# Kernel tuning notes

Hardware: AMD Instinct MI355X
Metric: run time of the kernel (lower is better)

## Reference

```python
import jax, jax.numpy as jnp
import numpy as np

B, C, Q, E = 32, 1024, 128, 512

def setup_inputs() -> dict:
    key = jax.random.key(0)
    k1, k2, k3 = jax.random.split(key, 3)
    context = jax.random.normal(k1, (B, C, E), dtype=jnp.float32)
    question = jax.random.normal(k2, (B, Q, E), dtype=jnp.float32)
    # ws = [ws_q | ws_c | ws_m], matching cat([q, ctx, q*ctx]) order
    ws = jax.random.normal(k3, (3 * E,), dtype=jnp.float32) * (1.0 / np.sqrt(E))
    return {"context": context, "question": question, "ws": ws}

def reference(context, question, ws):
    ws_q, ws_c, ws_m = ws[:E], ws[E:2 * E], ws[2 * E:]
    # similarity[b,c,q] = ws_q.q[b,q] + ws_c.c[b,c] + ws_m.(q[b,q]*c[b,c])
    sim = (jnp.einsum('bqe,e->bq', question, ws_q)[:, None, :]
           + jnp.einsum('bce,e->bc', context, ws_c)[:, :, None]
           + jnp.einsum('bce,bqe,e->bcq', context, question, ws_m))  # (B,C,Q)
    c2q = jnp.einsum('bcq,bqe->bce', jax.nn.softmax(sim, axis=2), question)  # (B,C,E)
    q2c_w = jax.nn.softmax(jnp.max(sim, axis=2), axis=1)  # (B,C)
    q2c = jnp.einsum('bc,bce->be', q2c_w, context)[:, None, :]  # (B,1,E)
    return (c2q, q2c)
```

## Files before the change

### kernel.cpp

```cpp
#include <hip/hip_runtime.h>

#define BB 32
#define CC 1024
#define QQ 128
#define EE 512

typedef unsigned int uint32;
typedef unsigned short u16;
typedef __bf16 bf16x8 __attribute__((ext_vector_type(8)));
typedef float f32x4 __attribute__((ext_vector_type(4)));

#define QMF_OFF  (0u)
#define QTF_OFF  (4u<<20)
#define QDP_OFF  (8u<<20)
#define MB_OFF   ((8u<<20)+(192u<<10))
#define SB_OFF   ((8u<<20)+(200u<<10))
#define PVB_OFF  ((8u<<20)+(256u<<10))
#define P_OFF    (13u<<20)

__device__ __forceinline__ u16 bfc(float f){
  __bf16 h = (__bf16)f;
  return __builtin_bit_cast(u16, h);
}
__device__ __forceinline__ float bf2f(uint32 lo16){
  return __builtin_bit_cast(float, lo16 << 16);
}

__global__ __launch_bounds__(256) void k_prep(const float* __restrict__ q,
                                              const float* __restrict__ ws,
                                              unsigned char* __restrict__ wsp){
  const int b = blockIdx.x >> 2, et = blockIdx.x & 3, e0 = et*128;
  __shared__ u16 tm[128*136];
  __shared__ u16 tt[128*136];
  const int tid = threadIdx.x;
  float* qdp = (float*)(wsp + QDP_OFF) + (size_t)(b*4 + et)*128;
  #pragma unroll
  for (int i=0;i<16;i++){
    int id = tid + i*256;
    int qi = id >> 5;
    int el = (id & 31) << 2;
    float4 v = *(const float4*)(q + (size_t)(b*QQ+qi)*EE + e0 + el);
    float4 a = *(const float4*)(ws +          e0 + el);
    float4 c = *(const float4*)(ws +   EE +   e0 + el);
    float4 m = *(const float4*)(ws + 2*EE +   e0 + el);
    ushort4 um; um.x = bfc(v.x*m.x + c.x); um.y = bfc(v.y*m.y + c.y);
                um.z = bfc(v.z*m.z + c.z); um.w = bfc(v.w*m.w + c.w);
    *(ushort4*)&tm[qi*136 + el] = um;
    ushort4 ut; ut.x = bfc(v.x); ut.y = bfc(v.y); ut.z = bfc(v.z); ut.w = bfc(v.w);
    *(ushort4*)&tt[qi*136 + el] = ut;
    float d = v.x*a.x + v.y*a.y + v.z*a.z + v.w*a.w;
    d += __shfl_xor(d,1); d += __shfl_xor(d,2); d += __shfl_xor(d,4);
    d += __shfl_xor(d,8); d += __shfl_xor(d,16);
    if ((tid & 31) == 0) qdp[qi] = d;
  }
  __syncthreads();
  const int lane = tid & 63, wv = tid >> 6, l15 = lane & 15, l4 = lane >> 4;
  uint4* qmf = (uint4*)(wsp + QMF_OFF);
  uint4* qtf = (uint4*)(wsp + QTF_OFF);
  #pragma unroll
  for (int i=0;i<8;i++){
    int f = wv*8 + i;
    int kl = f >> 3, nf = f & 7;
    uint4 u = *(const uint4*)&tm[(nf*16 + l15)*136 + kl*32 + l4*8];
    qmf[(size_t)((b*16 + et*4 + kl)*8 + nf)*64 + lane] = u;
  }
  #pragma unroll
  for (int i=0;i<8;i++){
    int f = wv*8 + i;
    int ks2 = f >> 3, nl = f & 7, ne = et*8 + nl;
    uint32 x[4];
    #pragma unroll
    for (int p=0;p<4;p++){
      u16 t0 = tt[(ks2*32 + l4*8 + 2*p    )*136 + nl*16 + l15];
      u16 t1 = tt[(ks2*32 + l4*8 + 2*p + 1)*136 + nl*16 + l15];
      x[p] = (uint32)t0 | ((uint32)t1 << 16);
    }
    uint4 u; u.x = x[0]; u.y = x[1]; u.z = x[2]; u.w = x[3];
    qtf[(size_t)((b*4 + ks2)*32 + ne)*64 + lane] = u;
  }
}

__global__ __launch_bounds__(512, 4) void k_sim(const float* __restrict__ ctx,
                                                unsigned char* __restrict__ wsp){
  __shared__ __align__(16) unsigned char buf[32768];
  __shared__ float mx_s[16*8];
  __shared__ float sm_s[16*8];
  __shared__ float wrow_s[16];

  const int bid = blockIdx.x;
  const int sw  = (bid & 7)*256 + (bid >> 3);
  const int b   = sw >> 6;
  const int t   = sw & 63;
  const int tid = threadIdx.x;
  const int lane = tid & 63;
  const int w    = tid >> 6;
  const int l15  = lane & 15;
  const int l4   = lane >> 4;

  {
    const unsigned char* cb = (const unsigned char*)(ctx + (size_t)(b*CC + t*16)*EE);
    #pragma unroll
    for (int j=0;j<4;j++){
      const int chunk = w*4 + j;
      const int row   = chunk >> 1;
      const int gs    = ((chunk & 1)*64 + lane) ^ (row & 7);
      __builtin_amdgcn_global_load_lds(
        (const __attribute__((address_space(1))) uint32*)(cb + row*2048 + gs*16),
        (__attribute__((address_space(3))) uint32*)(buf + chunk*1024 + lane*16),
        16, 0, 0);
    }
  }

  float qdv[4];
  {
    const float* qdp = (const float*)(wsp + QDP_OFF) + (size_t)b*512;
    #pragma unroll
    for (int r=0;r<4;r++){
      const int qi = w*16 + l4*4 + r;
      qdv[r] = qdp[qi] + qdp[128+qi] + qdp[256+qi] + qdp[384+qi];
    }
  }
  __syncthreads();

  const uint4* qmf4 = (const uint4*)(wsp + QMF_OFF);
  f32x4 acc = (f32x4){0.f,0.f,0.f,0.f};
  {
    const int swz = l15 & 7;
    const unsigned char* rowb = buf + l15*2048;
    #pragma unroll
    for (int ks=0; ks<16; ks++){
      bf16x8 a = __builtin_bit_cast(bf16x8, qmf4[(size_t)((b*16 + ks)*8 + w)*64 + lane]);
      const int gs0 = ks*8 + l4*2;
      float4 x = *(const float4*)(rowb + ((gs0    ) ^ swz)*16);
      float4 y = *(const float4*)(rowb + ((gs0 + 1) ^ swz)*16);
      bf16x8 bf;
      bf[0]=(__bf16)x.x; bf[1]=(__bf16)x.y; bf[2]=(__bf16)x.z; bf[3]=(__bf16)x.w;
      bf[4]=(__bf16)y.x; bf[5]=(__bf16)y.y; bf[6]=(__bf16)y.z; bf[7]=(__bf16)y.w;
      acc = __builtin_amdgcn_mfma_f32_16x16x32_bf16(a, bf, acc, 0, 0, 0);
    }
  }

  float p[4];
  {
    float m = -3.0e38f, s = 0.f;
    #pragma unroll
    for (int r=0;r<4;r++){
      float vv = fminf(acc[r] + qdv[r], 80.f);
      m = fmaxf(m, vv);
      p[r] = __expf(vv);
      s += p[r];
    }
    m = fmaxf(m, __shfl_xor(m, 16)); m = fmaxf(m, __shfl_xor(m, 32));
    s += __shfl_xor(s, 16);          s += __shfl_xor(s, 32);
    if (l4 == 0){ mx_s[l15*8 + w] = m; sm_s[l15*8 + w] = s; }
  }
  __syncthreads();

  {
    const float* sp = &sm_s[l15*8];
    const float rden = 1.f/(sp[0]+sp[1]+sp[2]+sp[3]+sp[4]+sp[5]+sp[6]+sp[7]);
    u16 hb[4];
    #pragma unroll
    for (int r=0;r<4;r++) hb[r] = bfc(p[r]*rden);
    uint2 u; u.x = (uint32)hb[0] | ((uint32)hb[1]<<16);
             u.y = (uint32)hb[2] | ((uint32)hb[3]<<16);
    *(uint2*)(wsp + P_OFF
      + ((size_t)(b*64 + t)*4 + (w>>1))*1024
      + (((2*w + (l4>>1)) & 3)*16 + l15)*16 + (l4&1)*8) = u;
  }

  if (tid < 16){
    const float* mp = &mx_s[tid*8];
    float mf = fmaxf(fmaxf(fmaxf(mp[0],mp[1]),fmaxf(mp[2],mp[3])),
                     fmaxf(fmaxf(mp[4],mp[5]),fmaxf(mp[6],mp[7])));
    float M = mf;
    M = fmaxf(M, __shfl_xor(M,1)); M = fmaxf(M, __shfl_xor(M,2));
    M = fmaxf(M, __shfl_xor(M,4)); M = fmaxf(M, __shfl_xor(M,8));
    float wr = __expf(mf - M);
    wrow_s[tid] = wr;
    float S = wr;
    S += __shfl_xor(S,1); S += __shfl_xor(S,2);
    S += __shfl_xor(S,4); S += __shfl_xor(S,8);
    if (tid == 0){
      ((float*)(wsp + MB_OFF))[b*64 + t] = M;
      ((float*)(wsp + SB_OFF))[b*64 + t] = S;
    }
  }
  __syncthreads();

  {
    const int sl = tid >> 2, in = (tid & 3)*4;
    float pv = 0.f;
    #pragma unroll
    for (int rr=0; rr<16; rr++){
      float x = *(const float*)(buf + rr*2048 + ((sl ^ (rr & 7))*16) + in);
      pv = fmaf(wrow_s[rr], x, pv);
    }
    ((float*)(wsp + PVB_OFF))[(size_t)(b*64 + t)*512 + tid] = pv;
  }
}

__global__ __launch_bounds__(256, 4) void k_out(unsigned char* __restrict__ wsp,
                                                float* __restrict__ out){
  __shared__ __align__(16) unsigned char qts[32768];
  __shared__ float sc_s[64];
  __shared__ float dinv_s;

  const int bid = blockIdx.x;
  const int tid = threadIdx.x;

  if (bid >= 2048){
    const int b = bid - 2048;
    if (tid < 64){
      float Mk = ((const float*)(wsp + MB_OFF))[b*64 + tid];
      float Sk = ((const float*)(wsp + SB_OFF))[b*64 + tid];
      float M = Mk;
      M = fmaxf(M, __shfl_xor(M,1));  M = fmaxf(M, __shfl_xor(M,2));
      M = fmaxf(M, __shfl_xor(M,4));  M = fmaxf(M, __shfl_xor(M,8));
      M = fmaxf(M, __shfl_xor(M,16)); M = fmaxf(M, __shfl_xor(M,32));
      float ev = __expf(Mk - M);
      float d = ev*Sk;
      d += __shfl_xor(d,1);  d += __shfl_xor(d,2);  d += __shfl_xor(d,4);
      d += __shfl_xor(d,8);  d += __shfl_xor(d,16); d += __shfl_xor(d,32);
      sc_s[tid] = ev;
      if (tid == 0) dinv_s = 1.f/d;
    }
    __syncthreads();
    const float* pvb = (const float*)(wsp + PVB_OFF) + (size_t)b*64*512;
    float a0 = 0.f, a1 = 0.f;
    #pragma unroll 8
    for (int k=0;k<64;k++){
      float s = sc_s[k];
      a0 = fmaf(s, pvb[(size_t)k*512 + tid],       a0);
      a1 = fmaf(s, pvb[(size_t)k*512 + tid + 256], a1);
    }
    size_t base = (size_t)BB*CC*EE + (size_t)b*EE;
    float di = dinv_s;
    out[base + tid]       = a0*di;
    out[base + tid + 256] = a1*di;
    return;
  }

  const int sw  = (bid & 7)*256 + (bid >> 3);
  const int b   = sw >> 6;
  const int rr  = sw & 63;
  const int ct  = rr >> 2;
  const int et  = rr & 3;
  const int lane = tid & 63;
  const int w    = tid >> 6;
  const int l15  = lane & 15;
  const int l4   = lane >> 4;

  const unsigned char* qtfb = wsp + QTF_OFF + (size_t)b*131072;
  #pragma unroll
  for (int j=0;j<8;j++){
    __builtin_amdgcn_global_load_lds(
      (const __attribute__((address_space(1))) uint32*)
        (qtfb + (size_t)(w*32 + et*8 + j)*1024 + lane*16),
      (__attribute__((address_space(3))) uint32*)(qts + (w*8 + j)*1024), 16, 0, 0);
  }

  bf16x8 pa[4];
  #pragma unroll
  for (int k2=0;k2<4;k2++)
    pa[k2] = __builtin_bit_cast(bf16x8,
      *(const uint4*)(wsp + P_OFF + ((size_t)(b*64 + ct*4 + w)*4 + k2)*1024 + lane*16));
  __syncthreads();

  f32x4 acc2[8];
  #pragma unroll
  for (int n=0;n<8;n++) acc2[n] = (f32x4){0.f,0.f,0.f,0.f};
  #pragma unroll
  for (int k2=0;k2<4;k2++){
    #pragma unroll
    for (int n=0;n<8;n++){
      bf16x8 bq = __builtin_bit_cast(bf16x8,
        *(const uint4*)(qts + (k2*8 + n)*1024 + lane*16));
      acc2[n] = __builtin_amdgcn_mfma_f32_16x16x32_bf16(pa[k2], bq, acc2[n], 0, 0, 0);
    }
  }

  float* ob = out + (size_t)(b*CC + ct*64 + w*16)*EE + et*128;
  #pragma unroll
  for (int n=0;n<8;n++){
    #pragma unroll
    for (int r=0;r<4;r++)
      ob[(size_t)(l4*4 + r)*EE + n*16 + l15] = acc2[n][r];
  }
}

extern "C" void kernel_launch(void* const* d_in, const int* in_sizes, int n_in,
                              void* d_out, int out_size, void* d_ws, size_t ws_size,
                              hipStream_t stream){
  const float* ctx = (const float*)d_in[0];
  const float* q   = (const float*)d_in[1];
  const float* ws  = (const float*)d_in[2];
  float* out = (float*)d_out;
  unsigned char* wsp = (unsigned char*)d_ws;

  k_prep<<<dim3(BB*4),    dim3(256), 0, stream>>>(q, ws, wsp);
  k_sim <<<dim3(2048),    dim3(512), 0, stream>>>(ctx, wsp);
  k_out <<<dim3(2048+32), dim3(256), 0, stream>>>(wsp, out);
}
```

Baseline: 53.09 us.

## Fuse similarity and output kernels into a flag-synchronized persistent megakernel

Replaces the separate similarity and output kernels with one persistent kernel of 256 blocks. 128 producer blocks loop over 16 context tiles each, double-buffering context loads into LDS, and publish a flag for every 4 tiles. 128 consumer blocks spin on those flags and compute c2q tiles plus the q2c reduction as soon as their rows are ready. The goal is to overlap the two phases and remove a launch boundary. The cost is far fewer in-flight blocks, serialized per-block work, spin-wait overhead, and reliance on producers and consumers being co-resident; a new zeroing kernel resets the flags.

New measurement: 121.0 us. +127.9%, slower.

```diff
diff --git a/kernel.cpp b/kernel.cpp
--- a/kernel.cpp
+++ b/kernel.cpp
@@ -15,6 +15,7 @@
 #define QDP_OFF  (8u<<20)
 #define MB_OFF   ((8u<<20)+(192u<<10))
 #define SB_OFF   ((8u<<20)+(200u<<10))
+#define FLG_OFF  ((8u<<20)+(208u<<10))
 #define PVB_OFF  ((8u<<20)+(256u<<10))
 #define P_OFF    (13u<<20)
 
@@ -24,6 +25,13 @@
 }
 __device__ __forceinline__ float bf2f(uint32 lo16){
   return __builtin_bit_cast(float, lo16 << 16);
+}
+__device__ __forceinline__ void flag_set(uint32* f){
+  __hip_atomic_store(f, 1u, __ATOMIC_RELEASE, __HIP_MEMORY_SCOPE_AGENT);
+}
+__device__ __forceinline__ void flag_wait(uint32* f){
+  while (__hip_atomic_load(f, __ATOMIC_ACQUIRE, __HIP_MEMORY_SCOPE_AGENT) == 0u)
+    __builtin_amdgcn_s_sleep(8);
 }
 
 __global__ __launch_bounds__(256) void k_prep(const float* __restrict__ q,
@@ -80,212 +88,230 @@
   }
 }
 
-__global__ __launch_bounds__(512, 4) void k_sim(const float* __restrict__ ctx,
-                                                unsigned char* __restrict__ wsp){
-  __shared__ __align__(16) unsigned char buf[32768];
+__global__ __launch_bounds__(512) void k_zero(unsigned char* __restrict__ wsp){
+  flag_set((uint32*)(wsp + FLG_OFF) + threadIdx.x),
+  __hip_atomic_store((uint32*)(wsp + FLG_OFF) + threadIdx.x, 0u,
+                     __ATOMIC_RELEASE, __HIP_MEMORY_SCOPE_AGENT);
+}
+
+__global__ __launch_bounds__(512) void k_mega(const float* __restrict__ ctx,
+                                              unsigned char* __restrict__ wsp,
+                                              float* __restrict__ out){
+  __shared__ __align__(16) unsigned char mega[65536];
   __shared__ float mx_s[16*8];
   __shared__ float sm_s[16*8];
   __shared__ float wrow_s[16];
+  __shared__ float sc_s[64];
+  __shared__ float dinv_s;
 
   const int bid = blockIdx.x;
-  const int sw  = (bid & 7)*256 + (bid >> 3);
-  const int b   = sw >> 6;
-  const int t   = sw & 63;
   const int tid = threadIdx.x;
   const int lane = tid & 63;
   const int w    = tid >> 6;
   const int l15  = lane & 15;
   const int l4   = lane >> 4;
-
-  {
-    const unsigned char* cb = (const unsigned char*)(ctx + (size_t)(b*CC + t*16)*EE);
+  uint32* flags = (uint32*)(wsp + FLG_OFF);
+
+  if (bid < 128){
+    const int b   = bid >> 2;
+    const int q16 = (bid & 3) * 16;
+
+    const uint4* qmf4 = (const uint4*)(wsp + QMF_OFF);
+    bf16x8 a[16];
     #pragma unroll
-    for (int j=0;j<4;j++){
-      const int chunk = w*4 + j;
-      const int row   = chunk >> 1;
-      const int gs    = ((chunk & 1)*64 + lane) ^ (row & 7);
+    for (int ks=0;ks<16;ks++)
+      a[ks] = __builtin_bit_cast(bf16x8, qmf4[(size_t)((b*16 + ks)*8 + w)*64 + lane]);
+    float qdv[4];
+    {
+      const float* qdp = (const float*)(wsp + QDP_OFF) + (size_t)b*512;
+      #pragma unroll
+      for (int r=0;r<4;r++){
+        const int qi = w*16 + l4*4 + r;
+        qdv[r] = qdp[qi] + qdp[128+qi] + qdp[256+qi] + qdp[384+qi];
+      }
+    }
+
+    auto stage = [&](int t, unsigned char* dst){
+      const unsigned char* cb = (const unsigned char*)(ctx + (size_t)(b*CC + t*16)*EE);
+      #pragma unroll
+      for (int j=0;j<4;j++){
+        const int chunk = w*4 + j;
+        const int row   = chunk >> 1;
+        const int gs    = ((chunk & 1)*64 + lane) ^ (row & 7);
+        __builtin_amdgcn_global_load_lds(
+          (const __attribute__((address_space(1))) uint32*)(cb + row*2048 + gs*16),
+          (__attribute__((address_space(3))) uint32*)(dst + chunk*1024 + lane*16),
+          16, 0, 0);
+      }
+    };
+
+    stage(q16, mega);
+    __syncthreads();
+
+    for (int it=0; it<16; ++it){
+      const int t = q16 + it;
+      unsigned char* bufc = mega + (it & 1)*32768;
+      if (it < 15) stage(t+1, mega + ((it & 1)^1)*32768);
+
+      f32x4 acc = (f32x4){0.f,0.f,0.f,0.f};
+      {
+        const int swz = l15 & 7;
+        const unsigned char* rowb = bufc + l15*2048;
+        #pragma unroll
+        for (int ks=0; ks<16; ks++){
+          const int gs0 = ks*8 + l4*2;
+          float4 x = *(const float4*)(rowb + ((gs0    ) ^ swz)*16);
+          float4 y = *(const float4*)(rowb + ((gs0 + 1) ^ swz)*16);
+          bf16x8 bf;
+          bf[0]=(__bf16)x.x; bf[1]=(__bf16)x.y; bf[2]=(__bf16)x.z; bf[3]=(__bf16)x.w;
+          bf[4]=(__bf16)y.x; bf[5]=(__bf16)y.y; bf[6]=(__bf16)y.z; bf[7]=(__bf16)y.w;
+          acc = __builtin_amdgcn_mfma_f32_16x16x32_bf16(a[ks], bf, acc, 0, 0, 0);
+        }
+      }
+
+      float p[4];
+      {
+        float m = -3.0e38f, s = 0.f;
+        #pragma unroll
+        for (int r=0;r<4;r++){
+          float vv = fminf(acc[r] + qdv[r], 80.f);
+          m = fmaxf(m, vv);
+          p[r] = __expf(vv);
+          s += p[r];
+        }
+        m = fmaxf(m, __shfl_xor(m, 16)); m = fmaxf(m, __shfl_xor(m, 32));
+        s += __shfl_xor(s, 16);          s += __shfl_xor(s, 32);
+        if (l4 == 0){ mx_s[l15*8 + w] = m; sm_s[l15*8 + w] = s; }
+      }
+      __syncthreads();
+
+      {
+        const float* sp = &sm_s[l15*8];
+        const float rden = 1.f/(sp[0]+sp[1]+sp[2]+sp[3]+sp[4]+sp[5]+sp[6]+sp[7]);
+        u16 hb[4];
+        #pragma unroll
+        for (int r=0;r<4;r++) hb[r] = bfc(p[r]*rden);
+        uint2 u; u.x = (uint32)hb[0] | ((uint32)hb[1]<<16);
+                 u.y = (uint32)hb[2] | ((uint32)hb[3]<<16);
+        *(uint2*)(wsp + P_OFF
+          + ((size_t)(b*64 + t)*4 + (w>>1))*1024
+          + (((2*w + (l4>>1)) & 3)*16 + l15)*16 + (l4&1)*8) = u;
+      }
+
+      if (tid < 16){
+        const float* mp = &mx_s[tid*8];
+        float mf = fmaxf(fmaxf(fmaxf(mp[0],mp[1]),fmaxf(mp[2],mp[3])),
+                         fmaxf(fmaxf(mp[4],mp[5]),fmaxf(mp[6],mp[7])));
+        float M = mf;
+        M = fmaxf(M, __shfl_xor(M,1)); M = fmaxf(M, __shfl_xor(M,2));
+        M = fmaxf(M, __shfl_xor(M,4)); M = fmaxf(M, __shfl_xor(M,8));
+        float wr = __expf(mf - M);
+        wrow_s[tid] = wr;
+        float S = wr;
+        S += __shfl_xor(S,1); S += __shfl_xor(S,2);
+        S += __shfl_xor(S,4); S += __shfl_xor(S,8);
+        if (tid == 0){
+          ((float*)(wsp + MB_OFF))[b*64 + t] = M;
+          ((float*)(wsp + SB_OFF))[b*64 + t] = S;
+        }
+      }
+      __syncthreads();
+
+      {
+        const int sl = tid >> 2, in = (tid & 3)*4;
+        float pv = 0.f;
+        #pragma unroll
+        for (int rr=0; rr<16; rr++){
+          float x = *(const float*)(bufc + rr*2048 + ((sl ^ (rr & 7))*16) + in);
+          pv = fmaf(wrow_s[rr], x, pv);
+        }
+        ((float*)(wsp + PVB_OFF))[(size_t)(b*64 + t)*512 + tid] = pv;
+      }
+      __syncthreads();
+
+      if ((it & 3) == 3 && tid == 0)
+        flag_set(flags + b*16 + (t >> 2));
+    }
+  } else {
+    const int c    = bid - 128;
+    const int b    = c >> 2;
+    const int half = c & 1;
+    const int ep   = (c >> 1) & 1;
+    const int g    = w >> 2;
+    const int wv4  = w & 3;
+    const int et   = ep*2 + g;
+
+    const unsigned char* qtfb = wsp + QTF_OFF + (size_t)b*131072;
+    #pragma unroll
+    for (int j=0;j<8;j++){
       __builtin_amdgcn_global_load_lds(
-        (const __attribute__((address_space(1))) uint32*)(cb + row*2048 + gs*16),
-        (__attribute__((address_space(3))) uint32*)(buf + chunk*1024 + lane*16),
+        (const __attribute__((address_space(1))) uint32*)
+          (qtfb + (size_t)(wv4*32 + et*8 + j)*1024 + lane*16),
+        (__attribute__((address_space(3))) uint32*)(mega + g*32768 + (wv4*8 + j)*1024 + lane*16),
         16, 0, 0);
     }
-  }
-
-  float qdv[4];
-  {
-    const float* qdp = (const float*)(wsp + QDP_OFF) + (size_t)b*512;
-    #pragma unroll
-    for (int r=0;r<4;r++){
-      const int qi = w*16 + l4*4 + r;
-      qdv[r] = qdp[qi] + qdp[128+qi] + qdp[256+qi] + qdp[384+qi];
-    }
-  }
-  __syncthreads();
-
-  const uint4* qmf4 = (const uint4*)(wsp + QMF_OFF);
-  f32x4 acc = (f32x4){0.f,0.f,0.f,0.f};
-  {
-    const int swz = l15 & 7;
-    const unsigned char* rowb = buf + l15*2048;
-    #pragma unroll
-    for (int ks=0; ks<16; ks++){
-      bf16x8 a = __builtin_bit_cast(bf16x8, qmf4[(size_t)((b*16 + ks)*8 + w)*64 + lane]);
-      const int gs0 = ks*8 + l4*2;
-      float4 x = *(const float4*)(rowb + ((gs0    ) ^ swz)*16);
-      float4 y = *(const float4*)(rowb + ((gs0 + 1) ^ swz)*16);
-      bf16x8 bf;
-      bf[0]=(__bf16)x.x; bf[1]=(__bf16)x.y; bf[2]=(__bf16)x.z; bf[3]=(__bf16)x.w;
-      bf[4]=(__bf16)y.x; bf[5]=(__bf16)y.y; bf[6]=(__bf16)y.z; bf[7]=(__bf16)y.w;
-      acc = __builtin_amdgcn_mfma_f32_16x16x32_bf16(a, bf, acc, 0, 0, 0);
-    }
-  }
-
-  float p[4];
-  {
-    float m = -3.0e38f, s = 0.f;
-    #pragma unroll
-    for (int r=0;r<4;r++){
-      float vv = fminf(acc[r] + qdv[r], 80.f);
-      m = fmaxf(m, vv);
-      p[r] = __expf(vv);
-      s += p[r];
-    }
-    m = fmaxf(m, __shfl_xor(m, 16)); m = fmaxf(m, __shfl_xor(m, 32));
-    s += __shfl_xor(s, 16);          s += __shfl_xor(s, 32);
-    if (l4 == 0){ mx_s[l15*8 + w] = m; sm_s[l15*8 + w] = s; }
-  }
-  __syncthreads();
-
-  {
-    const float* sp = &sm_s[l15*8];
-    const float rden = 1.f/(sp[0]+sp[1]+sp[2]+sp[3]+sp[4]+sp[5]+sp[6]+sp[7]);
-    u16 hb[4];
-    #pragma unroll
-    for (int r=0;r<4;r++) hb[r] = bfc(p[r]*rden);
-    uint2 u; u.x = (uint32)hb[0] | ((uint32)hb[1]<<16);
-             u.y = (uint32)hb[2] | ((uint32)hb[3]<<16);
-    *(uint2*)(wsp + P_OFF
-      + ((size_t)(b*64 + t)*4 + (w>>1))*1024
-      + (((2*w + (l4>>1)) & 3)*16 + l15)*16 + (l4&1)*8) = u;
-  }
-
-  if (tid < 16){
-    const float* mp = &mx_s[tid*8];
-    float mf = fmaxf(fmaxf(fmaxf(mp[0],mp[1]),fmaxf(mp[2],mp[3])),
-                     fmaxf(fmaxf(mp[4],mp[5]),fmaxf(mp[6],mp[7])));
-    float M = mf;
-    M = fmaxf(M, __shfl_xor(M,1)); M = fmaxf(M, __shfl_xor(M,2));
-    M = fmaxf(M, __shfl_xor(M,4)); M = fmaxf(M, __shfl_xor(M,8));
-    float wr = __expf(mf - M);
-    wrow_s[tid] = wr;
-    float S = wr;
-    S += __shfl_xor(S,1); S += __shfl_xor(S,2);
-    S += __shfl_xor(S,4); S += __shfl_xor(S,8);
-    if (tid == 0){
-      ((float*)(wsp + MB_OFF))[b*64 + t] = M;
-      ((float*)(wsp + SB_OFF))[b*64 + t] = S;
-    }
-  }
-  __syncthreads();
-
-  {
-    const int sl = tid >> 2, in = (tid & 3)*4;
-    float pv = 0.f;
-    #pragma unroll
-    for (int rr=0; rr<16; rr++){
-      float x = *(const float*)(buf + rr*2048 + ((sl ^ (rr & 7))*16) + in);
-      pv = fmaf(wrow_s[rr], x, pv);
-    }
-    ((float*)(wsp + PVB_OFF))[(size_t)(b*64 + t)*512 + tid] = pv;
-  }
-}
-
-__global__ __launch_bounds__(256, 4) void k_out(unsigned char* __restrict__ wsp,
-                                                float* __restrict__ out){
-  __shared__ __align__(16) unsigned char qts[32768];
-  __shared__ float sc_s[64];
-  __shared__ float dinv_s;
-
-  const int bid = blockIdx.x;
-  const int tid = threadIdx.x;
-
-  if (bid >= 2048){
-    const int b = bid - 2048;
-    if (tid < 64){
-      float Mk = ((const float*)(wsp + MB_OFF))[b*64 + tid];
-      float Sk = ((const float*)(wsp + SB_OFF))[b*64 + tid];
-      float M = Mk;
-      M = fmaxf(M, __shfl_xor(M,1));  M = fmaxf(M, __shfl_xor(M,2));
-      M = fmaxf(M, __shfl_xor(M,4));  M = fmaxf(M, __shfl_xor(M,8));
-      M = fmaxf(M, __shfl_xor(M,16)); M = fmaxf(M, __shfl_xor(M,32));
-      float ev = __expf(Mk - M);
-      float d = ev*Sk;
-      d += __shfl_xor(d,1);  d += __shfl_xor(d,2);  d += __shfl_xor(d,4);
-      d += __shfl_xor(d,8);  d += __shfl_xor(d,16); d += __shfl_xor(d,32);
-      sc_s[tid] = ev;
-      if (tid == 0) dinv_s = 1.f/d;
-    }
     __syncthreads();
-    const float* pvb = (const float*)(wsp + PVB_OFF) + (size_t)b*64*512;
-    float a0 = 0.f, a1 = 0.f;
-    #pragma unroll 8
-    for (int k=0;k<64;k++){
-      float s = sc_s[k];
-      a0 = fmaf(s, pvb[(size_t)k*512 + tid],       a0);
-      a1 = fmaf(s, pvb[(size_t)k*512 + tid + 256], a1);
-    }
-    size_t base = (size_t)BB*CC*EE + (size_t)b*EE;
-    float di = dinv_s;
-    out[base + tid]       = a0*di;
-    out[base + tid + 256] = a1*di;
-    return;
-  }
-
-  const int sw  = (bid & 7)*256 + (bid >> 3);
-  const int b   = sw >> 6;
-  const int rr  = sw & 63;
-  const int ct  = rr >> 2;
-  const int et  = rr & 3;
-  const int lane = tid & 63;
-  const int w    = tid >> 6;
-  const int l15  = lane & 15;
-  const int l4   = lane >> 4;
-
-  const unsigned char* qtfb = wsp + QTF_OFF + (size_t)b*131072;
-  #pragma unroll
-  for (int j=0;j<8;j++){
-    __builtin_amdgcn_global_load_lds(
-      (const __attribute__((address_space(1))) uint32*)
-        (qtfb + (size_t)(w*32 + et*8 + j)*1024 + lane*16),
-      (__attribute__((address_space(3))) uint32*)(qts + (w*8 + j)*1024), 16, 0, 0);
-  }
-
-  bf16x8 pa[4];
-  #pragma unroll
-  for (int k2=0;k2<4;k2++)
-    pa[k2] = __builtin_bit_cast(bf16x8,
-      *(const uint4*)(wsp + P_OFF + ((size_t)(b*64 + ct*4 + w)*4 + k2)*1024 + lane*16));
-  __syncthreads();
-
-  f32x4 acc2[8];
-  #pragma unroll
-  for (int n=0;n<8;n++) acc2[n] = (f32x4){0.f,0.f,0.f,0.f};
-  #pragma unroll
-  for (int k2=0;k2<4;k2++){
-    #pragma unroll
-    for (int n=0;n<8;n++){
-      bf16x8 bq = __builtin_bit_cast(bf16x8,
-        *(const uint4*)(qts + (k2*8 + n)*1024 + lane*16));
-      acc2[n] = __builtin_amdgcn_mfma_f32_16x16x32_bf16(pa[k2], bq, acc2[n], 0, 0, 0);
-    }
-  }
-
-  float* ob = out + (size_t)(b*CC + ct*64 + w*16)*EE + et*128;
-  #pragma unroll
-  for (int n=0;n<8;n++){
-    #pragma unroll
-    for (int r=0;r<4;r++)
-      ob[(size_t)(l4*4 + r)*EE + n*16 + l15] = acc2[n][r];
+
+    const unsigned char* qts = mega + g*32768;
+    for (int ih=0; ih<8; ++ih){
+      const int ct = half*8 + ih;
+      if (tid == 0) flag_wait(flags + b*16 + ct);
+      __syncthreads();
+
+      bf16x8 pa[4];
+      #pragma unroll
+      for (int k2=0;k2<4;k2++)
+        pa[k2] = __builtin_bit_cast(bf16x8,
+          *(const uint4*)(wsp + P_OFF + ((size_t)(b*64 + ct*4 + wv4)*4 + k2)*1024 + lane*16));
+
+      f32x4 acc2[8];
+      #pragma unroll
+      for (int n=0;n<8;n++) acc2[n] = (f32x4){0.f,0.f,0.f,0.f};
+      #pragma unroll
+      for (int k2=0;k2<4;k2++){
+        #pragma unroll
+        for (int n=0;n<8;n++){
+          bf16x8 bq = __builtin_bit_cast(bf16x8,
+            *(const uint4*)(qts + (k2*8 + n)*1024 + lane*16));
+          acc2[n] = __builtin_amdgcn_mfma_f32_16x16x32_bf16(pa[k2], bq, acc2[n], 0, 0, 0);
+        }
+      }
+      float* ob = out + (size_t)(b*CC + ct*64 + wv4*16)*EE + et*128;
+      #pragma unroll
+      for (int n=0;n<8;n++){
+        #pragma unroll
+        for (int r=0;r<4;r++)
+          ob[(size_t)(l4*4 + r)*EE + n*16 + l15] = acc2[n][r];
+      }
+    }
+
+    if ((c & 3) == 3){
+      if (tid == 0){
+        for (int i=0;i<8;i++) flag_wait(flags + b*16 + i);
+      }
+      __syncthreads();
+      if (tid < 64){
+        float Mk = ((const float*)(wsp + MB_OFF))[b*64 + tid];
+        float Sk = ((const float*)(wsp + SB_OFF))[b*64 + tid];
+        float M = Mk;
+        M = fmaxf(M, __shfl_xor(M,1));  M = fmaxf(M, __shfl_xor(M,2));
+        M = fmaxf(M, __shfl_xor(M,4));  M = fmaxf(M, __shfl_xor(M,8));
+        M = fmaxf(M, __shfl_xor(M,16)); M = fmaxf(M, __shfl_xor(M,32));
+        float ev = __expf(Mk - M);
+        float d = ev*Sk;
+        d += __shfl_xor(d,1);  d += __shfl_xor(d,2);  d += __shfl_xor(d,4);
+        d += __shfl_xor(d,8);  d += __shfl_xor(d,16); d += __shfl_xor(d,32);
+        sc_s[tid] = ev;
+        if (tid == 0) dinv_s = 1.f/d;
+      }
+      __syncthreads();
+      const float* pvb = (const float*)(wsp + PVB_OFF) + (size_t)b*64*512;
+      float a0 = 0.f;
+      #pragma unroll 8
+      for (int k=0;k<64;k++)
+        a0 = fmaf(sc_s[k], pvb[(size_t)k*512 + tid], a0);
+      out[(size_t)BB*CC*EE + (size_t)b*EE + tid] = a0*dinv_s;
+    }
   }
 }
 
@@ -298,7 +324,7 @@
   float* out = (float*)d_out;
   unsigned char* wsp = (unsigned char*)d_ws;
 
-  k_prep<<<dim3(BB*4),    dim3(256), 0, stream>>>(q, ws, wsp);
-  k_sim <<<dim3(2048),    dim3(512), 0, stream>>>(ctx, wsp);
-  k_out <<<dim3(2048+32), dim3(256), 0, stream>>>(wsp, out);
-}
+  k_prep<<<dim3(BB*4), dim3(256), 0, stream>>>(q, ws, wsp);
+  k_zero<<<dim3(1),    dim3(512), 0, stream>>>(wsp);
+  k_mega<<<dim3(256),  dim3(512), 0, stream>>>(ctx, wsp, out);
+}
```
